# Optimization experiments

Hardware: AMD Instinct MI355X
Metric: run time of the kernel (lower is better)

Reference implementation:

```python
import jax, jax.numpy as jnp
import numpy as np


def setup_inputs() -> dict:
    key = jax.random.key(0)
    k1, k2 = jax.random.split(key)
    B, D, H, W = 32, 64, 32, 32
    K = 1024
    z_e = jax.random.normal(k1, (B, D, H, W), dtype=jnp.float32)
    # original init: uniform(-1/K, 1/K); use same scale
    emb = jax.random.uniform(k2, (K, D), dtype=jnp.float32, minval=-1.0 / K, maxval=1.0 / K)
    return {"z_e": z_e, "emb": emb}


COMMITMENT_COST = 0.25


def reference(z_e, emb):
    # z_e: [B, D, H, W], emb: [K, D]
    B, D, H, W = z_e.shape
    K = emb.shape[0]
    z = jnp.transpose(z_e, (0, 2, 3, 1))           # [B, H, W, D]
    flat = z.reshape(-1, D)                        # [N, D]
    N = flat.shape[0]

    dist = (
        jnp.sum(flat * flat, axis=1, keepdims=True)
        + jnp.sum(emb * emb, axis=1)
        - 2.0 * flat @ emb.T
    )
    idx = jnp.argmin(dist, axis=1)                 # [N]
    encodings = jax.nn.one_hot(idx, K, dtype=flat.dtype)  # [N, K]
    z_q = (encodings @ emb).reshape(z.shape)       # [B, H, W, D]

    e_latent_loss = jnp.mean((jax.lax.stop_gradient(z_q) - z) ** 2)
    q_latent_loss = jnp.mean((z_q - jax.lax.stop_gradient(z)) ** 2)
    loss = q_latent_loss + COMMITMENT_COST * e_latent_loss

    # straight-through estimator
    z_st = z + jax.lax.stop_gradient(z_q - z)

    avg_probs = jnp.sum(encodings, axis=0) / jnp.float32(N)
    perplexity = jnp.exp(-jnp.sum(avg_probs * jnp.log(avg_probs + 1e-10)))

    return (jnp.transpose(z_st, (0, 3, 1, 2)), loss, perplexity, encodings)
```

## Files before the change

kernel.cpp:

```cpp
#include <hip/hip_runtime.h>
#include <stdint.h>
#include <math.h>

constexpr int Dd  = 64;
constexpr int Nn  = 32768;
constexpr int Kk  = 1024;

constexpr int OUT0_N   = 32 * 64 * 1024;
constexpr int OUT_LOSS = OUT0_N;
constexpr int OUT_PERP = OUT0_N + 1;
constexpr int OUT_ENC  = OUT0_N + 2;
constexpr int ENC_N    = Nn * Kk;
constexpr long long CAND_FLOAT_OFF = (long long)OUT_ENC + ENC_N - 2LL * 256 * 8 * 128;

constexpr size_t WS_LOSS = 0;
constexpr size_t WS_CNT  = 64;
constexpr size_t WS_BN   = WS_CNT + 4096;
constexpr size_t WS_AN   = WS_BN + 4096;
constexpr size_t WS_IDX  = WS_AN + 131072;

__global__ void norms_kernel(const float* __restrict__ z_e,
                             const float* __restrict__ emb,
                             float* __restrict__ An, float* __restrict__ Bn) {
#pragma clang fp contract(off)
    int t = blockIdx.x * blockDim.x + threadIdx.x;
    if (t < Nn) {
        int b = t >> 10, hw = t & 1023;
        const float* p = z_e + (size_t)b * 65536 + hw;
        float tt[64];
#pragma unroll
        for (int d = 0; d < 64; ++d) { float v = p[(size_t)d * 1024]; tt[d] = v * v; }
        float r[8];
#pragma unroll
        for (int j = 0; j < 8; ++j) r[j] = tt[j];
#pragma unroll
        for (int i = 8; i < 64; i += 8)
#pragma unroll
            for (int j = 0; j < 8; ++j) r[j] += tt[i + j];
        An[t] = ((r[0] + r[1]) + (r[2] + r[3])) + ((r[4] + r[5]) + (r[6] + r[7]));
    } else if (t < Nn + Kk) {
        int k = t - Nn;
        const float* p = emb + (size_t)k * 64;
        float tt[64];
#pragma unroll
        for (int d = 0; d < 64; ++d) { float v = p[d]; tt[d] = v * v; }
        float r[8];
#pragma unroll
        for (int j = 0; j < 8; ++j) r[j] = tt[j];
#pragma unroll
        for (int i = 8; i < 64; i += 8)
#pragma unroll
            for (int j = 0; j < 8; ++j) r[j] += tt[i + j];
        Bn[k] = ((r[0] + r[1]) + (r[2] + r[3])) + ((r[4] + r[5]) + (r[6] + r[7]));
    }
}

__device__ __forceinline__ uint32_t fsort(float f) {
    uint32_t b = __float_as_uint(f);
    return (b & 0x80000000u) ? ~b : (b | 0x80000000u);
}

__global__ __launch_bounds__(256, 2)
void dist_kernel(const float* __restrict__ z_e, const float* __restrict__ emb,
                 const float* __restrict__ An, const float* __restrict__ Bn,
                 unsigned long long* __restrict__ cand) {
    __shared__ float xs[128 * 68];
    __shared__ float es[128 * 68];
    const int tid = threadIdx.x;
    const int rg = blockIdx.x >> 3, cg = blockIdx.x & 7;
    const int n0 = rg * 128;
    const int b = n0 >> 10, hw0 = n0 & 1023;
    const float* zb = z_e + (size_t)b * 65536 + hw0;

    {
        int hwi = tid & 127;
        int d4g = tid >> 7;
#pragma unroll
        for (int it = 0; it < 8; ++it) {
            int dbase = (d4g + it * 2) * 4;
            float4 v;
            v.x = zb[(size_t)(dbase + 0) * 1024 + hwi];
            v.y = zb[(size_t)(dbase + 1) * 1024 + hwi];
            v.z = zb[(size_t)(dbase + 2) * 1024 + hwi];
            v.w = zb[(size_t)(dbase + 3) * 1024 + hwi];
            *(float4*)&xs[hwi * 68 + dbase] = v;
        }
    }
    {
        const float4* ep = (const float4*)(emb + (size_t)cg * 128 * 64);
#pragma unroll
        for (int it = 0; it < 8; ++it) {
            int j = tid + it * 256;
            float4 v = ep[j];
            int c = j >> 4, d4 = j & 15;
            *(float4*)&es[c * 68 + d4 * 4] = v;
        }
    }
    __syncthreads();

    const int tx = tid & 15, ty = tid >> 4;
    float acc[8][8];
#pragma unroll
    for (int i = 0; i < 8; ++i)
#pragma unroll
        for (int j = 0; j < 8; ++j) acc[i][j] = 0.0f;

#pragma unroll 1
    for (int d4 = 0; d4 < 16; ++d4) {
        float4 xv[8], ev[8];
#pragma unroll
        for (int i = 0; i < 8; ++i) xv[i] = *(const float4*)&xs[(ty + 16 * i) * 68 + d4 * 4];
#pragma unroll
        for (int j = 0; j < 8; ++j) ev[j] = *(const float4*)&es[(tx + 16 * j) * 68 + d4 * 4];
#pragma unroll
        for (int i = 0; i < 8; ++i)
#pragma unroll
            for (int j = 0; j < 8; ++j) {
                float a = acc[i][j];
                a = __builtin_fmaf(xv[i].x, ev[j].x, a);
                a = __builtin_fmaf(xv[i].y, ev[j].y, a);
                a = __builtin_fmaf(xv[i].z, ev[j].z, a);
                a = __builtin_fmaf(xv[i].w, ev[j].w, a);
                acc[i][j] = a;
            }
    }

    float Ar[8], Bc[8];
#pragma unroll
    for (int i = 0; i < 8; ++i) Ar[i] = An[n0 + ty + 16 * i];
#pragma unroll
    for (int j = 0; j < 8; ++j) Bc[j] = Bn[cg * 128 + tx + 16 * j];

    const size_t base = (size_t)blockIdx.x * 128;
#pragma unroll
    for (int i = 0; i < 8; ++i) {
        unsigned long long best = ~0ULL;
#pragma unroll
        for (int j = 0; j < 8; ++j) {
            float s = Ar[i] + Bc[j];
            float dist = s - 2.0f * acc[i][j];
            unsigned long long key = ((unsigned long long)fsort(dist) << 32)
                                   | (unsigned)(cg * 128 + tx + 16 * j);
            best = (key < best) ? key : best;
        }
#pragma unroll
        for (int m = 1; m < 16; m <<= 1) {
            unsigned long long o = __shfl_xor(best, m, 64);
            best = (o < best) ? o : best;
        }
        if (tx == 0) cand[base + ty + 16 * i] = best;
    }
}

__global__ void merge_kernel(const float* __restrict__ z_e,
                             const float* __restrict__ emb,
                             const unsigned long long* __restrict__ cand,
                             float* __restrict__ out0,
                             uint32_t* __restrict__ idx,
                             uint32_t* __restrict__ counts,
                             double* __restrict__ loss_sum) {
    int n = blockIdx.x * blockDim.x + threadIdx.x;
    int rg = n >> 7, r = n & 127;
    unsigned long long best = ~0ULL;
#pragma unroll
    for (int cg = 0; cg < 8; ++cg) {
        unsigned long long k = cand[((size_t)rg * 8 + cg) * 128 + r];
        best = (k < best) ? k : best;
    }
    uint32_t code = (uint32_t)best;
    idx[n] = code;
    atomicAdd(&counts[code], 1u);

    int b = n >> 10, hw = n & 1023;
    const float* zp = z_e + (size_t)b * 65536 + hw;
    float*       op = out0 + (size_t)b * 65536 + hw;
    const float* ep = emb + (size_t)code * 64;
    double ls = 0.0;
#pragma unroll
    for (int d = 0; d < 64; ++d) {
        float z  = zp[(size_t)d * 1024];
        float zq = ep[d];
        float t  = zq - z;
        op[(size_t)d * 1024] = z + t;
        ls += (double)t * (double)t;
    }
#pragma unroll
    for (int m = 32; m >= 1; m >>= 1) ls += __shfl_down(ls, m, 64);
    if ((threadIdx.x & 63) == 0) atomicAdd(loss_sum, ls);
}

__global__ void scalar_kernel(const uint32_t* __restrict__ counts,
                              const double* __restrict__ loss_sum,
                              float* __restrict__ out) {
    __shared__ double red[4];
    int t = threadIdx.x;
    double h = 0.0;
    for (int i = t; i < Kk; i += 256) {
        double p = (double)counts[i] * (1.0 / 32768.0);
        h += p * log(p + 1e-10);
    }
#pragma unroll
    for (int m = 32; m >= 1; m >>= 1) h += __shfl_down(h, m, 64);
    if ((t & 63) == 0) red[t >> 6] = h;
    __syncthreads();
    if (t == 0) {
        double H = red[0] + red[1] + red[2] + red[3];
        out[OUT_PERP] = (float)exp(-H);
        float m32 = (float)(loss_sum[0] * (1.0 / 2097152.0));
        out[OUT_LOSS] = m32 + 0.25f * m32;
    }
}

__global__ void enc_kernel(const uint32_t* __restrict__ idx,
                           float* __restrict__ enc) {
    int t = threadIdx.x;
#pragma unroll
    for (int i = 0; i < 4; ++i) {
        int row = blockIdx.x + i * 8192;
        uint32_t code = idx[row];
        float4 v;
        uint32_t c0 = (uint32_t)(t * 4);
        v.x = (code == c0 + 0u) ? 1.0f : 0.0f;
        v.y = (code == c0 + 1u) ? 1.0f : 0.0f;
        v.z = (code == c0 + 2u) ? 1.0f : 0.0f;
        v.w = (code == c0 + 3u) ? 1.0f : 0.0f;
        ((float4*)enc)[(size_t)row * 256 + t] = v;
    }
}

extern "C" void kernel_launch(void* const* d_in, const int* in_sizes, int n_in,
                              void* d_out, int out_size, void* d_ws, size_t ws_size,
                              hipStream_t stream) {
    const float* z_e = (const float*)d_in[0];
    const float* emb = (const float*)d_in[1];
    float* out = (float*)d_out;
    char* ws = (char*)d_ws;

    double*   loss_sum = (double*)(ws + WS_LOSS);
    uint32_t* counts   = (uint32_t*)(ws + WS_CNT);
    float*    Bn       = (float*)(ws + WS_BN);
    float*    An       = (float*)(ws + WS_AN);
    uint32_t* idx      = (uint32_t*)(ws + WS_IDX);
    unsigned long long* cand = (unsigned long long*)(out + CAND_FLOAT_OFF);

    hipMemsetAsync(ws, 0, WS_CNT + 4096, stream);

    norms_kernel<<<(Nn + Kk) / 256, 256, 0, stream>>>(z_e, emb, An, Bn);
    dist_kernel<<<2048, 256, 0, stream>>>(z_e, emb, An, Bn, cand);
    merge_kernel<<<Nn / 256, 256, 0, stream>>>(z_e, emb, cand, out, idx, counts, loss_sum);
    scalar_kernel<<<1, 256, 0, stream>>>(counts, loss_sum, out);
    enc_kernel<<<8192, 256, 0, stream>>>(idx, out + OUT_ENC);
}
```

Before: 242.3 us.

## Fuse norm computation into distance kernel and scalar reduction into encoding kernel

Removes the separate norms kernel: each dist block computes the row norms from its shared-memory tile and the 128 codebook norms directly from global memory. The codebook tile is no longer staged in shared memory, so each thread reads embedding float4s from global (L1/L2) inside the inner loop. The scalar perplexity/loss kernel is folded into block 0 of the encoding kernel. Together this cuts two kernel launches and reduces LDS use, at the cost of uncoalesced global embedding loads in the FMA loop and redundant norm computation per block.

```diff
diff --git a/kernel.cpp b/kernel.cpp
--- a/kernel.cpp
+++ b/kernel.cpp
@@ -2,7 +2,6 @@
 #include <stdint.h>
 #include <math.h>
 
-constexpr int Dd  = 64;
 constexpr int Nn  = 32768;
 constexpr int Kk  = 1024;
 
@@ -15,44 +14,27 @@
 
 constexpr size_t WS_LOSS = 0;
 constexpr size_t WS_CNT  = 64;
-constexpr size_t WS_BN   = WS_CNT + 4096;
-constexpr size_t WS_AN   = WS_BN + 4096;
-constexpr size_t WS_IDX  = WS_AN + 131072;
-
-__global__ void norms_kernel(const float* __restrict__ z_e,
-                             const float* __restrict__ emb,
-                             float* __restrict__ An, float* __restrict__ Bn) {
+constexpr size_t WS_IDX  = WS_CNT + 4096;
+
+__device__ __forceinline__ float norm64v(const float4* __restrict__ p) {
 #pragma clang fp contract(off)
-    int t = blockIdx.x * blockDim.x + threadIdx.x;
-    if (t < Nn) {
-        int b = t >> 10, hw = t & 1023;
-        const float* p = z_e + (size_t)b * 65536 + hw;
-        float tt[64];
-#pragma unroll
-        for (int d = 0; d < 64; ++d) { float v = p[(size_t)d * 1024]; tt[d] = v * v; }
-        float r[8];
-#pragma unroll
-        for (int j = 0; j < 8; ++j) r[j] = tt[j];
-#pragma unroll
-        for (int i = 8; i < 64; i += 8)
-#pragma unroll
-            for (int j = 0; j < 8; ++j) r[j] += tt[i + j];
-        An[t] = ((r[0] + r[1]) + (r[2] + r[3])) + ((r[4] + r[5]) + (r[6] + r[7]));
-    } else if (t < Nn + Kk) {
-        int k = t - Nn;
-        const float* p = emb + (size_t)k * 64;
-        float tt[64];
-#pragma unroll
-        for (int d = 0; d < 64; ++d) { float v = p[d]; tt[d] = v * v; }
-        float r[8];
-#pragma unroll
-        for (int j = 0; j < 8; ++j) r[j] = tt[j];
-#pragma unroll
-        for (int i = 8; i < 64; i += 8)
-#pragma unroll
-            for (int j = 0; j < 8; ++j) r[j] += tt[i + j];
-        Bn[k] = ((r[0] + r[1]) + (r[2] + r[3])) + ((r[4] + r[5]) + (r[6] + r[7]));
-    }
+    float tt[64];
+#pragma unroll
+    for (int q = 0; q < 16; ++q) {
+        float4 v = p[q];
+        tt[4 * q + 0] = v.x * v.x;
+        tt[4 * q + 1] = v.y * v.y;
+        tt[4 * q + 2] = v.z * v.z;
+        tt[4 * q + 3] = v.w * v.w;
+    }
+    float r[8];
+#pragma unroll
+    for (int j = 0; j < 8; ++j) r[j] = tt[j];
+#pragma unroll
+    for (int i = 8; i < 64; i += 8)
+#pragma unroll
+        for (int j = 0; j < 8; ++j) r[j] += tt[i + j];
+    return ((r[0] + r[1]) + (r[2] + r[3])) + ((r[4] + r[5]) + (r[6] + r[7]));
 }
 
 __device__ __forceinline__ uint32_t fsort(float f) {
@@ -62,10 +44,10 @@
 
 __global__ __launch_bounds__(256, 2)
 void dist_kernel(const float* __restrict__ z_e, const float* __restrict__ emb,
-                 const float* __restrict__ An, const float* __restrict__ Bn,
                  unsigned long long* __restrict__ cand) {
     __shared__ float xs[128 * 68];
-    __shared__ float es[128 * 68];
+    __shared__ float An_s[128];
+    __shared__ float Bn_s[128];
     const int tid = threadIdx.x;
     const int rg = blockIdx.x >> 3, cg = blockIdx.x & 7;
     const int n0 = rg * 128;
@@ -86,19 +68,19 @@
             *(float4*)&xs[hwi * 68 + dbase] = v;
         }
     }
-    {
-        const float4* ep = (const float4*)(emb + (size_t)cg * 128 * 64);
-#pragma unroll
-        for (int it = 0; it < 8; ++it) {
-            int j = tid + it * 256;
-            float4 v = ep[j];
-            int c = j >> 4, d4 = j & 15;
-            *(float4*)&es[c * 68 + d4 * 4] = v;
-        }
-    }
     __syncthreads();
 
+    if (tid < 128) {
+        An_s[tid] = norm64v((const float4*)&xs[tid * 68]);
+    } else {
+        int c = tid - 128;
+        Bn_s[c] = norm64v((const float4*)(emb + (size_t)(cg * 128 + c) * 64));
+    }
+    __syncthreads();
+
     const int tx = tid & 15, ty = tid >> 4;
+    const float4* ep = (const float4*)emb + (size_t)(cg * 128 + tx) * 16;
+
     float acc[8][8];
 #pragma unroll
     for (int i = 0; i < 8; ++i)
@@ -109,9 +91,9 @@
     for (int d4 = 0; d4 < 16; ++d4) {
         float4 xv[8], ev[8];
 #pragma unroll
+        for (int j = 0; j < 8; ++j) ev[j] = ep[(size_t)j * 256 + d4];
+#pragma unroll
         for (int i = 0; i < 8; ++i) xv[i] = *(const float4*)&xs[(ty + 16 * i) * 68 + d4 * 4];
-#pragma unroll
-        for (int j = 0; j < 8; ++j) ev[j] = *(const float4*)&es[(tx + 16 * j) * 68 + d4 * 4];
 #pragma unroll
         for (int i = 0; i < 8; ++i)
 #pragma unroll
@@ -127,9 +109,9 @@
 
     float Ar[8], Bc[8];
 #pragma unroll
-    for (int i = 0; i < 8; ++i) Ar[i] = An[n0 + ty + 16 * i];
-#pragma unroll
-    for (int j = 0; j < 8; ++j) Bc[j] = Bn[cg * 128 + tx + 16 * j];
+    for (int i = 0; i < 8; ++i) Ar[i] = An_s[ty + 16 * i];
+#pragma unroll
+    for (int j = 0; j < 8; ++j) Bc[j] = Bn_s[tx + 16 * j];
 
     const size_t base = (size_t)blockIdx.x * 128;
 #pragma unroll
@@ -189,30 +171,11 @@
     if ((threadIdx.x & 63) == 0) atomicAdd(loss_sum, ls);
 }
 
-__global__ void scalar_kernel(const uint32_t* __restrict__ counts,
-                              const double* __restrict__ loss_sum,
-                              float* __restrict__ out) {
-    __shared__ double red[4];
-    int t = threadIdx.x;
-    double h = 0.0;
-    for (int i = t; i < Kk; i += 256) {
-        double p = (double)counts[i] * (1.0 / 32768.0);
-        h += p * log(p + 1e-10);
-    }
-#pragma unroll
-    for (int m = 32; m >= 1; m >>= 1) h += __shfl_down(h, m, 64);
-    if ((t & 63) == 0) red[t >> 6] = h;
-    __syncthreads();
-    if (t == 0) {
-        double H = red[0] + red[1] + red[2] + red[3];
-        out[OUT_PERP] = (float)exp(-H);
-        float m32 = (float)(loss_sum[0] * (1.0 / 2097152.0));
-        out[OUT_LOSS] = m32 + 0.25f * m32;
-    }
-}
-
 __global__ void enc_kernel(const uint32_t* __restrict__ idx,
-                           float* __restrict__ enc) {
+                           const uint32_t* __restrict__ counts,
+                           const double* __restrict__ loss_sum,
+                           float* __restrict__ out) {
+    float* enc = out + OUT_ENC;
     int t = threadIdx.x;
 #pragma unroll
     for (int i = 0; i < 4; ++i) {
@@ -226,6 +189,24 @@
         v.w = (code == c0 + 3u) ? 1.0f : 0.0f;
         ((float4*)enc)[(size_t)row * 256 + t] = v;
     }
+    if (blockIdx.x == 0) {
+        __shared__ double red[4];
+        double h = 0.0;
+        for (int i = t; i < Kk; i += 256) {
+            double p = (double)counts[i] * (1.0 / 32768.0);
+            h += p * log(p + 1e-10);
+        }
+#pragma unroll
+        for (int m = 32; m >= 1; m >>= 1) h += __shfl_down(h, m, 64);
+        if ((t & 63) == 0) red[t >> 6] = h;
+        __syncthreads();
+        if (t == 0) {
+            double H = red[0] + red[1] + red[2] + red[3];
+            out[OUT_PERP] = (float)exp(-H);
+            float m32 = (float)(loss_sum[0] * (1.0 / 2097152.0));
+            out[OUT_LOSS] = m32 + 0.25f * m32;
+        }
+    }
 }
 
 extern "C" void kernel_launch(void* const* d_in, const int* in_sizes, int n_in,
@@ -238,16 +219,12 @@
 
     double*   loss_sum = (double*)(ws + WS_LOSS);
     uint32_t* counts   = (uint32_t*)(ws + WS_CNT);
-    float*    Bn       = (float*)(ws + WS_BN);
-    float*    An       = (float*)(ws + WS_AN);
     uint32_t* idx      = (uint32_t*)(ws + WS_IDX);
     unsigned long long* cand = (unsigned long long*)(out + CAND_FLOAT_OFF);
 
     hipMemsetAsync(ws, 0, WS_CNT + 4096, stream);
 
-    norms_kernel<<<(Nn + Kk) / 256, 256, 0, stream>>>(z_e, emb, An, Bn);
-    dist_kernel<<<2048, 256, 0, stream>>>(z_e, emb, An, Bn, cand);
+    dist_kernel<<<2048, 256, 0, stream>>>(z_e, emb, cand);
     merge_kernel<<<Nn / 256, 256, 0, stream>>>(z_e, emb, cand, out, idx, counts, loss_sum);
-    scalar_kernel<<<1, 256, 0, stream>>>(counts, loss_sum, out);
-    enc_kernel<<<8192, 256, 0, stream>>>(idx, out + OUT_ENC);
-}
+    enc_kernel<<<8192, 256, 0, stream>>>(idx, counts, loss_sum, out);
+}
```

Result: slower. 303.9 us (+25.4%).
